# Kernel tuning notes

Hardware: AMD Instinct MI355X
Metric: run time of the kernel (lower is better)

Reference implementation:

```python
import jax, jax.numpy as jnp
import numpy as np

H, D = 16, 64  # num_attention_heads, attention_head_size
BASE = 10000.0

def _rope(q, k, seq_len):
    # RotaryPositionalEmbedding: inv_freq over arange(0, D, 2); emb = cat(freqs, freqs)
    inv_freq = 1.0 / (BASE ** (jnp.arange(0, D, 2, dtype=jnp.float32) / D))  # [D/2]=32
    pos = jnp.arange(seq_len, dtype=jnp.float32)
    freqs = jnp.outer(pos, inv_freq)            # [S, 32]; equals cos_emb[..., :d]
    cos, sin = jnp.cos(freqs), jnp.sin(freqs)   # [S, 32]
    d = D // 2                                   # 32: only first half of head dim rotated
    half = d // 2                                # 16: internal rotate-half within rot part
    def rot(x):  # x: [B, H, S, D]
        xr, xp = x[..., :d], x[..., d:]
        swapped = jnp.concatenate([xr[..., half:], xr[..., :half]], axis=-1)
        xr2 = xr * cos - swapped * sin
        return jnp.concatenate([xr2, xp], axis=-1)
    return rot(q), rot(k)

def setup_inputs() -> dict:
    key = jax.random.key(0)
    ks = jax.random.split(key, 9)
    B, S, E = 2, 2048, 1024
    std = 0.02  # initializer_range
    inp = {"hidden_states": jax.random.normal(ks[0], (B, S, E), jnp.float32)}
    for i, n in enumerate(["q", "k", "v", "d"]):
        inp[f"W{n}"] = jax.random.normal(ks[1 + 2 * i], (E, E), jnp.float32) * std
        inp[f"b{n}"] = jnp.zeros((E,), jnp.float32)
    return inp

def reference(hidden_states, Wq, bq, Wk, bk, Wv, bv, Wd, bd):
    B, S, E = hidden_states.shape
    def heads(x):  # [B,S,E] -> [B,H,S,D]
        return x.reshape(B, S, H, D).transpose(0, 2, 1, 3)
    q = heads(hidden_states @ Wq + bq)
    k = heads(hidden_states @ Wk + bk)
    v = heads(hidden_states @ Wv + bv)
    q, k = _rope(q, k, S)
    scores = jnp.einsum("bhqd,bhkd->bhqk", q, k) / jnp.sqrt(jnp.float32(D))
    causal = jnp.tril(jnp.ones((S, S), dtype=bool))
    scores = jnp.where(causal, scores, -jnp.inf)
    probs = jax.nn.softmax(scores, axis=-1)
    ctx = jnp.einsum("bhqk,bhkd->bhqd", probs, v)
    ctx = ctx.transpose(0, 2, 1, 3).reshape(B, S, E)
    return ctx @ Wd + bd
```

## Files before the change

kernel.cpp:

```cpp
#include <hip/hip_runtime.h>
#include <stdint.h>

typedef __bf16 bf8 __attribute__((ext_vector_type(8)));
typedef float f4 __attribute__((ext_vector_type(4)));
typedef float f16v __attribute__((ext_vector_type(16)));
typedef unsigned short us8 __attribute__((ext_vector_type(8)));
typedef unsigned short us4 __attribute__((ext_vector_type(4)));

#define MFMA16(a, b, c) __builtin_amdgcn_mfma_f32_16x16x32_bf16(a, b, c, 0, 0, 0)
#define MFMA32(a, b, c) __builtin_amdgcn_mfma_f32_32x32x16_bf16(a, b, c, 0, 0, 0)

__device__ __forceinline__ unsigned short f2b(float f) {
  union { float f; unsigned u; } x; x.f = f;
  unsigned u = x.u;
  u += 0x7fffu + ((u >> 16) & 1u);
  return (unsigned short)(u >> 16);
}

__device__ __forceinline__ unsigned pk2(float a, float b) {
  union { float f; unsigned u; } ua, ub; ua.f = a; ub.f = b;
  return __builtin_amdgcn_perm(ub.u + 0x8000u, ua.u + 0x8000u, 0x07060302u);
}

__device__ __forceinline__ void gload16(const void* g, void* l) {
  __builtin_amdgcn_global_load_lds(
      (const __attribute__((address_space(1))) void*)g,
      (__attribute__((address_space(3))) void*)l, 16, 0, 0);
}

__global__ __launch_bounds__(256) void prep_kernel(
    const float* __restrict__ W0, const float* __restrict__ W1,
    const float* __restrict__ W2, const float* __restrict__ W3,
    unsigned short* __restrict__ T0, unsigned short* __restrict__ T1,
    unsigned short* __restrict__ T2, unsigned short* __restrict__ T3,
    const float* __restrict__ hid, unsigned short* __restrict__ hb) {
  if (blockIdx.z == 4) {
    int bi = blockIdx.x + 32 * blockIdx.y;
#pragma unroll
    for (int k = 0; k < 4; ++k) {
      int i = bi * 1024 + k * 256 + threadIdx.x;
      float4 v = ((const float4*)hid)[i];
      us4 r = { f2b(v.x), f2b(v.y), f2b(v.z), f2b(v.w) };
      *(us4*)(hb + (size_t)i * 4) = r;
    }
    return;
  }
  const float* W; unsigned short* Wt;
  if (blockIdx.z == 0)      { W = W0; Wt = T0; }
  else if (blockIdx.z == 1) { W = W1; Wt = T1; }
  else if (blockIdx.z == 2) { W = W2; Wt = T2; }
  else                      { W = W3; Wt = T3; }
  __shared__ float tile[32][33];
  int tx = threadIdx.x & 31, ty = threadIdx.x >> 5;
  int kb = blockIdx.x * 32, nb = blockIdx.y * 32;
#pragma unroll
  for (int j = 0; j < 32; j += 8)
    tile[ty + j][tx] = W[(size_t)(kb + ty + j) * 1024 + nb + tx];
  __syncthreads();
#pragma unroll
  for (int j = 0; j < 32; j += 8)
    Wt[(size_t)(nb + ty + j) * 1024 + kb + tx] = f2b(tile[tx][ty + j]);
}

__global__ __launch_bounds__(256) void gemm_qkv_kernel(
    const unsigned short* __restrict__ X,
    const unsigned short* __restrict__ Wqt, const unsigned short* __restrict__ Wkt,
    const unsigned short* __restrict__ Wvt,
    const float* __restrict__ bq, const float* __restrict__ bk,
    const float* __restrict__ bv,
    unsigned short* __restrict__ Qo, unsigned short* __restrict__ Ko,
    unsigned short* __restrict__ Vo) {
  const unsigned short* Wt; const float* bias; unsigned short* out;
  if (blockIdx.z == 0)      { Wt = Wqt; bias = bq; out = Qo; }
  else if (blockIdx.z == 1) { Wt = Wkt; bias = bk; out = Ko; }
  else                      { Wt = Wvt; bias = bv; out = Vo; }

  __shared__ unsigned short As[128 * 32];
  __shared__ unsigned short Bs[128 * 32];
  const int t = threadIdx.x;
  const int wave = t >> 6, lane = t & 63, quad = lane >> 4, l16 = lane & 15;
  const int wm = (wave >> 1) * 64, wn = (wave & 1) * 64;
  const int m0 = blockIdx.y * 128, n0 = blockIdx.x * 128;

  f4 acc[4][4];
#pragma unroll
  for (int mi = 0; mi < 4; ++mi)
#pragma unroll
    for (int ni = 0; ni < 4; ++ni) acc[mi][ni] = (f4)0.0f;

  for (int k0 = 0; k0 < 1024; k0 += 32) {
    __syncthreads();
#pragma unroll
    for (int it = 0; it < 2; ++it) {
      int chunk = it * 256 + wave * 64 + lane;
      int row = chunk >> 2, c = chunk & 3;
      gload16(&X[(size_t)(m0 + row) * 1024 + k0 + c * 8],
              &As[(size_t)(it * 256 + wave * 64) * 8]);
      gload16(&Wt[(size_t)(n0 + row) * 1024 + k0 + c * 8],
              &Bs[(size_t)(it * 256 + wave * 64) * 8]);
    }
    __syncthreads();
    bf8 a[4], b[4];
#pragma unroll
    for (int mi = 0; mi < 4; ++mi)
      a[mi] = *(const bf8*)&As[(wm + mi * 16 + l16) * 32 + quad * 8];
#pragma unroll
    for (int ni = 0; ni < 4; ++ni)
      b[ni] = *(const bf8*)&Bs[(wn + ni * 16 + l16) * 32 + quad * 8];
#pragma unroll
    for (int mi = 0; mi < 4; ++mi)
#pragma unroll
      for (int ni = 0; ni < 4; ++ni)
        acc[mi][ni] = MFMA16(a[mi], b[ni], acc[mi][ni]);
  }

  float biasv[4];
#pragma unroll
  for (int ni = 0; ni < 4; ++ni) biasv[ni] = bias[n0 + wn + ni * 16 + l16];

  if (blockIdx.z < 2) {
    const float kr = 13.287712379549449f / 32.0f;
    const float f0 = exp2f(-(float)l16 * kr);
    const float f1 = exp2f(-(float)(l16 + 16) * kr);
    const float qs = (blockIdx.z == 0) ? 0.18033688011112042f : 1.0f;
#pragma unroll
    for (int mi = 0; mi < 4; ++mi) {
#pragma unroll
      for (int r = 0; r < 4; ++r) {
        int m = m0 + wm + mi * 16 + quad * 4 + r;
        float s = (float)(m & 2047);
        float s0, c0, s1, c1;
        __sincosf(s * f0, &s0, &c0);
        __sincosf(s * f1, &s1, &c1);
        float v0 = acc[mi][0][r] + biasv[0];
        float v1 = acc[mi][1][r] + biasv[1];
        acc[mi][0][r] = (v0 * c0 - v1 * s0) * qs;
        acc[mi][1][r] = (v1 * c1 - v0 * s1) * qs;
        acc[mi][2][r] = (acc[mi][2][r] + biasv[2]) * qs;
        acc[mi][3][r] = (acc[mi][3][r] + biasv[3]) * qs;
      }
    }
#pragma unroll
    for (int ni = 0; ni < 4; ++ni) {
      int n = n0 + wn + ni * 16 + l16;
      int h = n >> 6, d = n & 63;
#pragma unroll
      for (int mi = 0; mi < 4; ++mi) {
#pragma unroll
        for (int r = 0; r < 4; ++r) {
          int m = m0 + wm + mi * 16 + quad * 4 + r;
          int b_ = m >> 11, s = m & 2047;
          out[(size_t)(((b_ << 4) | h) * 2048 + s) * 64 + d] = f2b(acc[mi][ni][r]);
        }
      }
    }
  } else {
#pragma unroll
    for (int ni = 0; ni < 4; ++ni) {
      int n = n0 + wn + ni * 16 + l16;
      int h = n >> 6, d = n & 63;
#pragma unroll
      for (int mi = 0; mi < 4; ++mi) {
        int m = m0 + wm + mi * 16 + quad * 4;
        int b_ = m >> 11, s = m & 2047;
        us4 w = { f2b(acc[mi][ni][0] + biasv[ni]), f2b(acc[mi][ni][1] + biasv[ni]),
                  f2b(acc[mi][ni][2] + biasv[ni]), f2b(acc[mi][ni][3] + biasv[ni]) };
        *(us4*)&out[((size_t)(((b_ << 4) | h) * 64 + d)) * 2048 + s] = w;
      }
    }
  }
}

__global__ __launch_bounds__(256, 2) void flash_attn_kernel(
    const unsigned short* __restrict__ Q, const unsigned short* __restrict__ K,
    const unsigned short* __restrict__ Vt, unsigned short* __restrict__ ctx) {
  __shared__ float Mrg[2][64][34];

  const int t = threadIdx.x;
  const int lane = t & 63;
  const int wave = t >> 6, l32 = lane & 31, hl = lane >> 5;
  const int qsub = wave >> 1, khalf = wave & 1;

  const int id = blockIdx.x;
  const int bh = id & 31;
  const int j = id >> 5;
  const int g = (j < 16) ? j : 47 - j;
  const int qbase = g * 64;
  const int b = bh >> 4, h = bh & 15;

  const unsigned short* Qh = Q + (size_t)bh * 2048 * 64;
  const unsigned short* Kh = K + (size_t)bh * 2048 * 64;
  const unsigned short* Vh = Vt + (size_t)bh * 64 * 2048;

  const int wrow0 = qbase + qsub * 32;
  const int q = wrow0 + l32;

  bf8 qb[4];
#pragma unroll
  for (int c = 0; c < 4; ++c)
    qb[c] = *(const bf8*)&Qh[(size_t)q * 64 + c * 16 + hl * 8];

  f16v o0 = (f16v)0.0f, o1 = (f16v)0.0f;
  float mrow = -3e38f, lrow = 0.0f;

  bf8 kf[2][4], vf[2][4];

  for (int kt = khalf; kt <= g; kt += 2) {
    const int k0 = kt * 64;
#pragma unroll
    for (int mt = 0; mt < 2; ++mt)
#pragma unroll
      for (int c = 0; c < 4; ++c)
        kf[mt][c] = *(const bf8*)&Kh[(size_t)(k0 + mt * 32 + l32) * 64 + c * 16 + hl * 8];
#pragma unroll
    for (int dt = 0; dt < 2; ++dt)
#pragma unroll
      for (int c = 0; c < 4; ++c)
        vf[dt][c] = *(const bf8*)&Vh[(size_t)(dt * 32 + l32) * 2048 + k0 + c * 16 + hl * 8];

    f16v s0 = (f16v)0.0f, s1 = (f16v)0.0f;
#pragma unroll
    for (int c = 0; c < 4; ++c) {
      s0 = MFMA32(kf[0][c], qb[c], s0);
      s1 = MFMA32(kf[1][c], qb[c], s1);
    }
    if (k0 + 64 > wrow0) {
#pragma unroll
      for (int gg = 0; gg < 4; ++gg)
#pragma unroll
        for (int i = 0; i < 4; ++i) {
          int kk = k0 + gg * 8 + hl * 4 + i;
          if (kk > q) s0[gg * 4 + i] = -3e38f;
          if (kk + 32 > q) s1[gg * 4 + i] = -3e38f;
        }
    }
    float mx = fmaxf(s0[0], s1[0]);
#pragma unroll
    for (int i = 1; i < 16; ++i) mx = fmaxf(mx, fmaxf(s0[i], s1[i]));
    mx = fmaxf(mx, __shfl_xor(mx, 32));
    float mn = fmaxf(mrow, mx);
    float al = exp2f(mrow - mn);
    mrow = mn;
    uint2 pd2[8];
    float sum = 0.0f;
#pragma unroll
    for (int gg = 0; gg < 4; ++gg) {
      float p0 = exp2f(s0[gg * 4 + 0] - mn), p1 = exp2f(s0[gg * 4 + 1] - mn);
      float p2 = exp2f(s0[gg * 4 + 2] - mn), p3 = exp2f(s0[gg * 4 + 3] - mn);
      sum += (p0 + p1) + (p2 + p3);
      pd2[gg].x = pk2(p0, p1); pd2[gg].y = pk2(p2, p3);
      float r0 = exp2f(s1[gg * 4 + 0] - mn), r1 = exp2f(s1[gg * 4 + 1] - mn);
      float r2 = exp2f(s1[gg * 4 + 2] - mn), r3 = exp2f(s1[gg * 4 + 3] - mn);
      sum += (r0 + r1) + (r2 + r3);
      pd2[4 + gg].x = pk2(r0, r1); pd2[4 + gg].y = pk2(r2, r3);
    }
#pragma unroll
    for (int i = 0; i < 16; ++i) { o0[i] *= al; o1[i] *= al; }
#pragma unroll
    for (int c = 0; c < 4; ++c) {
      uint2 lo = pd2[2 * c], hi = pd2[2 * c + 1];
      unsigned sx = hl ? lo.x : hi.x, sy = hl ? lo.y : hi.y;
      unsigned rx = __shfl_xor(sx, 32), ry = __shfl_xor(sy, 32);
      union { uint4 u; bf8 v; } fr;
      fr.u.x = hl ? rx : lo.x;
      fr.u.y = hl ? ry : lo.y;
      fr.u.z = hl ? hi.x : rx;
      fr.u.w = hl ? hi.y : ry;
      o0 = MFMA32(vf[0][c], fr.v, o0);
      o1 = MFMA32(vf[1][c], fr.v, o1);
    }
    sum += __shfl_xor(sum, 32);
    lrow = lrow * al + sum;
  }

  if (khalf == 1) {
#pragma unroll
    for (int i = 0; i < 16; ++i) {
      Mrg[qsub][lane][i] = o0[i];
      Mrg[qsub][lane][16 + i] = o1[i];
    }
    Mrg[qsub][lane][32] = mrow;
    Mrg[qsub][lane][33] = lrow;
  }
  __syncthreads();
  if (khalf == 0) {
    float m1 = Mrg[qsub][lane][32], l1 = Mrg[qsub][lane][33];
    float mm = fmaxf(mrow, m1);
    float a0 = exp2f(mrow - mm), a1 = exp2f(m1 - mm);
    float inv = 1.0f / (lrow * a0 + l1 * a1);
    a0 *= inv; a1 *= inv;
#pragma unroll
    for (int gg = 0; gg < 4; ++gg) {
      int d0 = gg * 8 + hl * 4;
      us4 w0 = { f2b(o0[gg * 4 + 0] * a0 + Mrg[qsub][lane][gg * 4 + 0] * a1),
                 f2b(o0[gg * 4 + 1] * a0 + Mrg[qsub][lane][gg * 4 + 1] * a1),
                 f2b(o0[gg * 4 + 2] * a0 + Mrg[qsub][lane][gg * 4 + 2] * a1),
                 f2b(o0[gg * 4 + 3] * a0 + Mrg[qsub][lane][gg * 4 + 3] * a1) };
      *(us4*)&ctx[((size_t)(b * 2048 + q)) * 1024 + h * 64 + d0] = w0;
      us4 w1 = { f2b(o1[gg * 4 + 0] * a0 + Mrg[qsub][lane][16 + gg * 4 + 0] * a1),
                 f2b(o1[gg * 4 + 1] * a0 + Mrg[qsub][lane][16 + gg * 4 + 1] * a1),
                 f2b(o1[gg * 4 + 2] * a0 + Mrg[qsub][lane][16 + gg * 4 + 2] * a1),
                 f2b(o1[gg * 4 + 3] * a0 + Mrg[qsub][lane][16 + gg * 4 + 3] * a1) };
      *(us4*)&ctx[((size_t)(b * 2048 + q)) * 1024 + h * 64 + 32 + d0] = w1;
    }
  }
}

__global__ __launch_bounds__(256) void gemm_out_kernel(
    const unsigned short* __restrict__ A,
    const unsigned short* __restrict__ Wt,
    const float* __restrict__ bias, float* __restrict__ out) {
  __shared__ unsigned short As[64 * 32];
  __shared__ unsigned short Bs[128 * 32];
  const int t = threadIdx.x;
  const int wave = t >> 6, lane = t & 63, quad = lane >> 4, l16 = lane & 15;
  const int wm = (wave & 1) * 32, wn = (wave >> 1) * 64;
  const int m0 = blockIdx.y * 64, n0 = blockIdx.x * 128;

  f4 acc[2][4];
#pragma unroll
  for (int mi = 0; mi < 2; ++mi)
#pragma unroll
    for (int ni = 0; ni < 4; ++ni) acc[mi][ni] = (f4)0.0f;

  for (int k0 = 0; k0 < 1024; k0 += 32) {
    __syncthreads();
    {
      int chunk = wave * 64 + lane;
      int row = chunk >> 2, c = chunk & 3;
      gload16(&A[(size_t)(m0 + row) * 1024 + k0 + c * 8],
              &As[(size_t)(wave * 64) * 8]);
#pragma unroll
      for (int it = 0; it < 2; ++it) {
        int ch = it * 256 + wave * 64 + lane;
        int rw = ch >> 2, cc = ch & 3;
        gload16(&Wt[(size_t)(n0 + rw) * 1024 + k0 + cc * 8],
                &Bs[(size_t)(it * 256 + wave * 64) * 8]);
      }
    }
    __syncthreads();
    bf8 a[2], b[4];
#pragma unroll
    for (int mi = 0; mi < 2; ++mi)
      a[mi] = *(const bf8*)&As[(wm + mi * 16 + l16) * 32 + quad * 8];
#pragma unroll
    for (int ni = 0; ni < 4; ++ni)
      b[ni] = *(const bf8*)&Bs[(wn + ni * 16 + l16) * 32 + quad * 8];
#pragma unroll
    for (int mi = 0; mi < 2; ++mi)
#pragma unroll
      for (int ni = 0; ni < 4; ++ni)
        acc[mi][ni] = MFMA16(a[mi], b[ni], acc[mi][ni]);
  }
#pragma unroll
  for (int ni = 0; ni < 4; ++ni) {
    int n = n0 + wn + ni * 16 + l16;
    float bv_ = bias[n];
#pragma unroll
    for (int mi = 0; mi < 2; ++mi) {
#pragma unroll
      for (int r = 0; r < 4; ++r) {
        int m = m0 + wm + mi * 16 + quad * 4 + r;
        out[(size_t)m * 1024 + n] = acc[mi][ni][r] + bv_;
      }
    }
  }
}

extern "C" void kernel_launch(void* const* d_in, const int* in_sizes, int n_in,
                              void* d_out, int out_size, void* d_ws, size_t ws_size,
                              hipStream_t stream) {
  const float* hidden = (const float*)d_in[0];
  const float* Wq = (const float*)d_in[1];
  const float* bq = (const float*)d_in[2];
  const float* Wk = (const float*)d_in[3];
  const float* bk = (const float*)d_in[4];
  const float* Wv = (const float*)d_in[5];
  const float* bv = (const float*)d_in[6];
  const float* Wd = (const float*)d_in[7];
  const float* bd = (const float*)d_in[8];
  float* out = (float*)d_out;

  char* ws = (char*)d_ws;
  unsigned short* Xb  = (unsigned short*)(ws);
  unsigned short* Wqt = (unsigned short*)(ws + ( 8ull << 20));
  unsigned short* Wkt = (unsigned short*)(ws + (10ull << 20));
  unsigned short* Wvt = (unsigned short*)(ws + (12ull << 20));
  unsigned short* Wdt = (unsigned short*)(ws + (14ull << 20));
  unsigned short* Qb  = (unsigned short*)(ws + (16ull << 20));
  unsigned short* Kb  = (unsigned short*)(ws + (24ull << 20));
  unsigned short* Vb  = (unsigned short*)(ws + (32ull << 20));
  unsigned short* Cb  = (unsigned short*)(ws + (40ull << 20));

  prep_kernel<<<dim3(32, 32, 5), 256, 0, stream>>>(
      Wq, Wk, Wv, Wd, Wqt, Wkt, Wvt, Wdt, hidden, Xb);
  gemm_qkv_kernel<<<dim3(8, 32, 3), 256, 0, stream>>>(
      Xb, Wqt, Wkt, Wvt, bq, bk, bv, Qb, Kb, Vb);
  flash_attn_kernel<<<1024, 256, 0, stream>>>(Qb, Kb, Vb, Cb);
  gemm_out_kernel<<<dim3(8, 64), 256, 0, stream>>>(Cb, Wdt, bd, out);
}
```

Measured before the change: 224.3 us.

## Give each flash-attention wave its own query rows instead of split-K merging

The attention kernel now assigns 128 query rows per block, with each of the four waves owning 32 rows and iterating over all causal key tiles alone. This replaces the old scheme where pairs of waves split the key range and merged partial softmax results through shared memory. The shared-memory merge and its block barrier go away, and the grid shrinks from 1024 to 512 blocks. In exchange, each wave runs a longer serial loop, waves within a block have uneven causal work, and there are fewer blocks available to balance load across the GPU.

```diff
diff --git a/kernel.cpp b/kernel.cpp
--- a/kernel.cpp
+++ b/kernel.cpp
@@ -174,25 +174,22 @@
 __global__ __launch_bounds__(256, 2) void flash_attn_kernel(
     const unsigned short* __restrict__ Q, const unsigned short* __restrict__ K,
     const unsigned short* __restrict__ Vt, unsigned short* __restrict__ ctx) {
-  __shared__ float Mrg[2][64][34];
-
   const int t = threadIdx.x;
   const int lane = t & 63;
   const int wave = t >> 6, l32 = lane & 31, hl = lane >> 5;
-  const int qsub = wave >> 1, khalf = wave & 1;
 
   const int id = blockIdx.x;
-  const int bh = id & 31;
-  const int j = id >> 5;
-  const int g = (j < 16) ? j : 47 - j;
-  const int qbase = g * 64;
+  const int p = id & 255, sbit = id >> 8;
+  const int qt = p >> 4;
+  const int bh = ((p & 15) << 1) | sbit;
+  const int qbase = qt * 128;
   const int b = bh >> 4, h = bh & 15;
 
   const unsigned short* Qh = Q + (size_t)bh * 2048 * 64;
   const unsigned short* Kh = K + (size_t)bh * 2048 * 64;
   const unsigned short* Vh = Vt + (size_t)bh * 64 * 2048;
 
-  const int wrow0 = qbase + qsub * 32;
+  const int wrow0 = qbase + wave * 32;
   const int q = wrow0 + l32;
 
   bf8 qb[4];
@@ -204,8 +201,9 @@
   float mrow = -3e38f, lrow = 0.0f;
 
   bf8 kf[2][4], vf[2][4];
-
-  for (int kt = khalf; kt <= g; kt += 2) {
+  const int nkw = (wrow0 >> 6) + 1;
+
+  for (int kt = 0; kt < nkw; ++kt) {
     const int k0 = kt * 64;
 #pragma unroll
     for (int mt = 0; mt < 2; ++mt)
@@ -273,36 +271,16 @@
     lrow = lrow * al + sum;
   }
 
-  if (khalf == 1) {
-#pragma unroll
-    for (int i = 0; i < 16; ++i) {
-      Mrg[qsub][lane][i] = o0[i];
-      Mrg[qsub][lane][16 + i] = o1[i];
-    }
-    Mrg[qsub][lane][32] = mrow;
-    Mrg[qsub][lane][33] = lrow;
-  }
-  __syncthreads();
-  if (khalf == 0) {
-    float m1 = Mrg[qsub][lane][32], l1 = Mrg[qsub][lane][33];
-    float mm = fmaxf(mrow, m1);
-    float a0 = exp2f(mrow - mm), a1 = exp2f(m1 - mm);
-    float inv = 1.0f / (lrow * a0 + l1 * a1);
-    a0 *= inv; a1 *= inv;
-#pragma unroll
-    for (int gg = 0; gg < 4; ++gg) {
-      int d0 = gg * 8 + hl * 4;
-      us4 w0 = { f2b(o0[gg * 4 + 0] * a0 + Mrg[qsub][lane][gg * 4 + 0] * a1),
-                 f2b(o0[gg * 4 + 1] * a0 + Mrg[qsub][lane][gg * 4 + 1] * a1),
-                 f2b(o0[gg * 4 + 2] * a0 + Mrg[qsub][lane][gg * 4 + 2] * a1),
-                 f2b(o0[gg * 4 + 3] * a0 + Mrg[qsub][lane][gg * 4 + 3] * a1) };
-      *(us4*)&ctx[((size_t)(b * 2048 + q)) * 1024 + h * 64 + d0] = w0;
-      us4 w1 = { f2b(o1[gg * 4 + 0] * a0 + Mrg[qsub][lane][16 + gg * 4 + 0] * a1),
-                 f2b(o1[gg * 4 + 1] * a0 + Mrg[qsub][lane][16 + gg * 4 + 1] * a1),
-                 f2b(o1[gg * 4 + 2] * a0 + Mrg[qsub][lane][16 + gg * 4 + 2] * a1),
-                 f2b(o1[gg * 4 + 3] * a0 + Mrg[qsub][lane][16 + gg * 4 + 3] * a1) };
-      *(us4*)&ctx[((size_t)(b * 2048 + q)) * 1024 + h * 64 + 32 + d0] = w1;
-    }
+  float inv = 1.0f / lrow;
+#pragma unroll
+  for (int gg = 0; gg < 4; ++gg) {
+    int d0 = gg * 8 + hl * 4;
+    us4 w0 = { f2b(o0[gg * 4 + 0] * inv), f2b(o0[gg * 4 + 1] * inv),
+               f2b(o0[gg * 4 + 2] * inv), f2b(o0[gg * 4 + 3] * inv) };
+    *(us4*)&ctx[((size_t)(b * 2048 + q)) * 1024 + h * 64 + d0] = w0;
+    us4 w1 = { f2b(o1[gg * 4 + 0] * inv), f2b(o1[gg * 4 + 1] * inv),
+               f2b(o1[gg * 4 + 2] * inv), f2b(o1[gg * 4 + 3] * inv) };
+    *(us4*)&ctx[((size_t)(b * 2048 + q)) * 1024 + h * 64 + 32 + d0] = w1;
   }
 }
 
@@ -396,6 +374,6 @@
       Wq, Wk, Wv, Wd, Wqt, Wkt, Wvt, Wdt, hidden, Xb);
   gemm_qkv_kernel<<<dim3(8, 32, 3), 256, 0, stream>>>(
       Xb, Wqt, Wkt, Wvt, bq, bk, bv, Qb, Kb, Vb);
-  flash_attn_kernel<<<1024, 256, 0, stream>>>(Qb, Kb, Vb, Cb);
+  flash_attn_kernel<<<512, 256, 0, stream>>>(Qb, Kb, Vb, Cb);
   gemm_out_kernel<<<dim3(8, 64), 256, 0, stream>>>(Cb, Wdt, bd, out);
 }
```

Result: slower. 273.7 us (+22.1%).
